# Kernel optimization log

Measured on AMD Instinct MI355X. Metric: run time of the kernel, lower is better.

## Reference

```python
import jax, jax.numpy as jnp
import numpy as np

B, N, D, H, DH = 2, 2048, 1024, 16, 64  # batch, seq, dim, heads, dim_head


def setup_inputs() -> dict:
    key = jax.random.key(0)
    ks = jax.random.split(key, 5)
    x = jax.random.normal(ks[0], (B, N, D), dtype=jnp.float32)
    Wq = jax.random.normal(ks[1], (D, H * DH), dtype=jnp.float32) * 0.02
    Wk = jax.random.normal(ks[2], (D, H * DH), dtype=jnp.float32) * 0.02
    Wv = jax.random.normal(ks[3], (D, H * DH), dtype=jnp.float32) * 0.02
    Wo = jax.random.normal(ks[4], (H * DH, D), dtype=jnp.float32) * 0.02
    bo = jnp.zeros((D,), dtype=jnp.float32)
    return {"x": x, "Wq": Wq, "Wk": Wk, "Wv": Wv, "Wo": Wo, "bo": bo}


def reference(x, Wq, Wk, Wv, Wo, bo):
    b, n, _ = x.shape
    scale = DH ** -0.5
    q = (x @ Wq).reshape(b, n, H, DH)
    k = (x @ Wk).reshape(b, n, H, DH)
    v = (x @ Wv).reshape(b, n, H, DH)
    # ALiBi slopes: 1 / (256**(1/H))**(h+1), per get_alibi_slope
    base = (2.0 ** 8) ** (1.0 / H)
    slope = 1.0 / base ** jnp.arange(1, H + 1, dtype=jnp.float32)  # [H]
    pos = jnp.arange(n, dtype=jnp.float32)
    # q_bias=[slope, slope*i], k_bias=[-j, 1] -> dot = slope*(i-j)
    bias = slope[:, None, None] * (pos[:, None] - pos[None, :])  # [H, N, N]
    scores = jnp.einsum('bihd,bjhd->bhij', q, k) * scale + bias[None]
    causal = pos[:, None] >= pos[None, :]  # i >= j
    scores = jnp.where(causal[None, None], scores, jnp.float32(-1e30))
    attn = jax.nn.softmax(scores, axis=-1)
    out = jnp.einsum('bhij,bjhd->bihd', attn, v).reshape(b, n, H * DH)
    return out @ Wo + bo
```

## Files before the change

kernel.cpp:

```cpp
#include <hip/hip_runtime.h>
#include <hip/hip_bf16.h>


typedef __bf16 bf16x8 __attribute__((ext_vector_type(8)));
typedef float f32x4 __attribute__((ext_vector_type(4)));
typedef short s4 __attribute__((ext_vector_type(4)));
typedef unsigned short ushort_t;

#define MFMA_16x16x32(a, b, c) __builtin_amdgcn_mfma_f32_16x16x32_bf16(a, b, c, 0, 0, 0)
#define MFMA16(a, b, c) __builtin_amdgcn_mfma_f32_16x16x16bf16_1k(a, b, c, 0, 0, 0)

__device__ __forceinline__ ushort_t f2bf(float f) {
    __hip_bfloat16 h = __float2bfloat16(f);
    return __builtin_bit_cast(ushort_t, h);
}
__device__ __forceinline__ float bf2f(ushort_t u) {
    unsigned x = ((unsigned)u) << 16;
    return __builtin_bit_cast(float, x);
}

__device__ __forceinline__ void gl_lds16(const ushort_t* g, ushort_t* l) {
    __builtin_amdgcn_global_load_lds(
        (const __attribute__((address_space(1))) void*)g,
        (__attribute__((address_space(3))) void*)l, 16, 0, 0);
}

__device__ __forceinline__ unsigned detect_fp32(const void* wp) {
    const ushort_t* w = (const ushort_t*)wp;
    unsigned c = 0;
    #pragma unroll
    for (int i = 0; i < 128; ++i) c += (((w[i] >> 7) & 0xFF) >= 0x7F) ? 1u : 0u;
    return (c > 8) ? 1u : 0u;
}

__device__ __forceinline__ uint4 load8(const void* p, size_t idx, unsigned flag) {
    if (flag) {
        const float* f = (const float*)p + idx;
        float4 a = *(const float4*)f;
        float4 b = *(const float4*)(f + 4);
        ushort_t u[8] = { f2bf(a.x), f2bf(a.y), f2bf(a.z), f2bf(a.w),
                          f2bf(b.x), f2bf(b.y), f2bf(b.z), f2bf(b.w) };
        return *(uint4*)u;
    }
    return *(const uint4*)((const ushort_t*)p + idx);
}

struct Sched { unsigned v[1536]; unsigned short pair[238]; };
constexpr Sched make_sched() {
    Sched s{};
    for (int i = 0; i < 1536; ++i) s.v[i] = 0;
    int jc[16] = {1, 1, 2, 2, 3, 4, 6, 8, 12, 16, 23, 32, 32, 32, 32, 32};
    int grp[8][4] = {
        {11, 12, 0, 2}, {13, 14, 1, 3}, {27, 28, 16, 18}, {29, 30, 17, 19},
        {15, 10, 5, 4}, {31, 26, 21, 20}, {9, 8, 7, 6}, {25, 24, 23, 22},
    };
    int np = 0;
    for (int x = 0; x < 8; ++x) {
        int sb_bh[200], sb_qb[200], sb_jb[200], sb_je[200], sb_kd[200], sb_k[200];
        int n = 0;
        for (int gi = 0; gi < 4; ++gi) {
            int bh = grp[x][gi], h = bh & 15;
            for (int qb = 0; qb < 32; ++qb) {
                int w = (qb + 1 < jc[h]) ? (qb + 1) : jc[h];
                if (w >= 16) {
                    int k = np++;
                    s.pair[k] = (unsigned short)((qb << 5) | bh);
                    int jm = w / 2;
                    sb_bh[n] = bh; sb_qb[n] = qb; sb_jb[n] = 0;  sb_je[n] = jm; sb_kd[n] = 2; sb_k[n] = k; ++n;
                    sb_bh[n] = bh; sb_qb[n] = qb; sb_jb[n] = jm; sb_je[n] = w;  sb_kd[n] = 3; sb_k[n] = k; ++n;
                } else {
                    sb_bh[n] = bh; sb_qb[n] = qb; sb_jb[n] = 0; sb_je[n] = w; sb_kd[n] = 1; sb_k[n] = 0; ++n;
                }
            }
        }
        int m = 0;
        for (int w = 16; w >= 1; --w)
            for (int i2 = 0; i2 < n; ++i2)
                if (sb_je[i2] - sb_jb[i2] == w) {
                    int t = m++;
                    int r = t >> 5, p = t & 31;
                    int cu = (r & 1) ? (31 - p) : p;
                    s.v[r * 256 + cu * 8 + x] = (unsigned)(
                        sb_kd[i2] | (sb_bh[i2] << 2) | (sb_qb[i2] << 7) |
                        (sb_jb[i2] << 12) | (sb_je[i2] << 17) | (sb_k[i2] << 23));
                }
    }
    return s;
}
__constant__ Sched g_sched = make_sched();

__global__ __launch_bounds__(256) void convert_x(
    const void* __restrict__ X, const void* __restrict__ Wq, const void* __restrict__ bo,
    ushort_t* __restrict__ Xc, ushort_t* __restrict__ boc)
{
    const unsigned flag = detect_fp32(Wq);
    const int blk = blockIdx.x;
    if (blk < 2048) {
        size_t idx = (size_t)blk * 2048 + (size_t)threadIdx.x * 8;
        *(uint4*)(Xc + idx) = load8(X, idx, flag);
    } else {
        size_t idx = (size_t)threadIdx.x * 8;
        if (idx < 1024) *(uint4*)(boc + idx) = load8(bo, idx, flag);
    }
}

__global__ __launch_bounds__(256) void transpose_w(
    const void* __restrict__ Wq, const void* __restrict__ Wk,
    const void* __restrict__ Wv, const void* __restrict__ Wo,
    ushort_t* __restrict__ WqT, ushort_t* __restrict__ WkT,
    ushort_t* __restrict__ WvT, ushort_t* __restrict__ WoT)
{
    __shared__ ushort_t T[64][72];
    const unsigned flag = detect_fp32(Wq);
    const int z = blockIdx.z;
    const void* W = (z == 0) ? Wq : ((z == 1) ? Wk : ((z == 2) ? Wv : Wo));
    ushort_t* WT = (z == 0) ? WqT : ((z == 1) ? WkT : ((z == 2) ? WvT : WoT));

    const int k0 = blockIdx.y * 64, n0 = blockIdx.x * 64;
    const int r = threadIdx.x >> 2, c = (threadIdx.x & 3) * 16;

    *(uint4*)&T[r][c]     = load8(W, (size_t)(k0 + r) * 1024 + n0 + c,     flag);
    *(uint4*)&T[r][c + 8] = load8(W, (size_t)(k0 + r) * 1024 + n0 + c + 8, flag);
    __syncthreads();
    ushort_t tmp[16];
    #pragma unroll
    for (int j = 0; j < 16; ++j) tmp[j] = T[c + j][r];
    *(uint4*)(WT + (size_t)(n0 + r) * 1024 + k0 + c)     = *(uint4*)&tmp[0];
    *(uint4*)(WT + (size_t)(n0 + r) * 1024 + k0 + c + 8) = *(uint4*)&tmp[8];
}

__global__ __launch_bounds__(256) void qkv_gemm(
    const ushort_t* __restrict__ X, const ushort_t* __restrict__ WqT,
    const ushort_t* __restrict__ WkT, const ushort_t* __restrict__ WvT,
    ushort_t* __restrict__ Q, ushort_t* __restrict__ K, ushort_t* __restrict__ Vt)
{
    __shared__ ushort_t As[128 * 32];
    __shared__ ushort_t Bs[128 * 32];

    const int z = blockIdx.z;
    const ushort_t* WT = (z == 0) ? WqT : ((z == 1) ? WkT : WvT);

    const int tid  = threadIdx.x;
    const int m0   = blockIdx.y * 128, n0 = blockIdx.x * 128;
    const int lane = tid & 63, wv = tid >> 6;
    const int quad = lane >> 4, l15 = lane & 15;
    const int wm = (wv & 1) * 64, wn = (wv >> 1) * 64;

    const int lrow = lane >> 2;
    const int schk = (lane & 3) ^ ((lane >> 3) & 3);
    const int ra0_ = wv * 16 + lrow;
    ushort_t* aB0 = As + wv * 512;
    ushort_t* aB1 = As + 2048 + wv * 512;
    ushort_t* bB0 = Bs + wv * 512;
    ushort_t* bB1 = Bs + 2048 + wv * 512;
    const int sp = quad ^ ((l15 >> 1) & 3);

    f32x4 acc[4][4] = {};

    for (int kt = 0; kt < 32; ++kt) {
        const int k0 = kt * 32;
        __syncthreads();
        gl_lds16(X  + (size_t)(m0 + ra0_)      * 1024 + k0 + schk * 8, aB0);
        gl_lds16(X  + (size_t)(m0 + 64 + ra0_) * 1024 + k0 + schk * 8, aB1);
        gl_lds16(WT + (size_t)(n0 + ra0_)      * 1024 + k0 + schk * 8, bB0);
        gl_lds16(WT + (size_t)(n0 + 64 + ra0_) * 1024 + k0 + schk * 8, bB1);
        __syncthreads();

        bf16x8 af[4], bfr[4];
        #pragma unroll
        for (int t = 0; t < 4; ++t) {
            af[t]  = *(const bf16x8*)(As + (wm + t * 16 + l15) * 32 + sp * 8);
            bfr[t] = *(const bf16x8*)(Bs + (wn + t * 16 + l15) * 32 + sp * 8);
        }
        #pragma unroll
        for (int mt = 0; mt < 4; ++mt)
            #pragma unroll
            for (int nt = 0; nt < 4; ++nt)
                acc[mt][nt] = MFMA_16x16x32(af[mt], bfr[nt], acc[mt][nt]);
    }

    #pragma unroll
    for (int mt = 0; mt < 4; ++mt) {
        #pragma unroll
        for (int nt = 0; nt < 4; ++nt) {
            if (z == 2) {
                int c  = n0 + wn + nt * 16 + l15;
                int h  = c >> 6, dh = c & 63;
                int mA = m0 + wm + mt * 16 + quad * 4;
                int b  = mA >> 11, nseq = mA & 2047;
                ushort_t pk[4];
                #pragma unroll
                for (int r = 0; r < 4; ++r) pk[r] = f2bf(acc[mt][nt][r]);
                *(ushort2*)(Vt + ((size_t)((b * 16 + h) * 64 + dh)) * 2048 + nseq)     = *(ushort2*)&pk[0];
                *(ushort2*)(Vt + ((size_t)((b * 16 + h) * 64 + dh)) * 2048 + nseq + 2) = *(ushort2*)&pk[2];
            } else {
                ushort_t* dst = (z == 0) ? Q : K;
                #pragma unroll
                for (int r = 0; r < 4; ++r) {
                    int m = m0 + wm + mt * 16 + quad * 4 + r;
                    int c = n0 + wn + nt * 16 + l15;
                    int b = m >> 11, nseq = m & 2047;
                    int h = c >> 6, dh = c & 63;
                    dst[((size_t)((b * 16 + h) * 2048 + nseq)) * 64 + dh] = f2bf(acc[mt][nt][r]);
                }
            }
        }
    }
}

__global__ __launch_bounds__(256) void attn_kernel(
    const ushort_t* __restrict__ Q, const ushort_t* __restrict__ K,
    const ushort_t* __restrict__ Vt, ushort_t* __restrict__ AO,
    float* __restrict__ partV, float* __restrict__ partL)
{
    __shared__ ushort_t Ks[64 * 72];
    __shared__ ushort_t Vs[64 * 72];

    const unsigned e = g_sched.v[blockIdx.x];
    const int kind = e & 3;
    if (kind == 0) return;

    const int tid  = threadIdx.x;
    const int wv   = tid >> 6, lane = tid & 63;
    const int quad = lane >> 4, l15 = lane & 15;
    const int bh   = (e >> 2) & 31, h = bh & 15, b = bh >> 4;
    const int qb   = (e >> 7) & 31;
    const int jbeg = (e >> 12) & 31;
    const int jend = (e >> 17) & 63;
    const int pk_  = (e >> 23) & 255;
    const int iw   = qb * 64 + wv * 16;
    const int i_   = iw + l15;

    const ushort_t* Qh = Q  + (size_t)bh * 2048 * 64;
    const ushort_t* Kh = K  + (size_t)bh * 2048 * 64;
    const ushort_t* Vh = Vt + (size_t)bh * 64 * 2048;

    const float LOG2E = 1.44269504088896340736f;
    const float sl2 = exp2f(-0.5f * (float)(h + 1)) * LOG2E;
    const float c1  = 0.125f * LOG2E;

    bf16x8 qf0 = *(const bf16x8*)(Qh + (size_t)(iw + l15) * 64 + quad * 8);
    bf16x8 qf1 = *(const bf16x8*)(Qh + (size_t)(iw + l15) * 64 + 32 + quad * 8);

    s4 onesf;
    #pragma unroll
    for (int e2 = 0; e2 < 4; ++e2) onesf[e2] = (short)0x3F80;

    float nb[4];
    #pragma unroll
    for (int r = 0; r < 4; ++r) nb[r] = -sl2 * (float)(quad * 4 + r);

    f32x4 accv[4] = {};
    f32x4 accl = {};

    const int sr = tid >> 2, sc = (tid & 3) * 16;

    const int j0b = jbeg * 64;
    uint4 ka0 = *(const uint4*)(Kh + (size_t)(j0b + sr) * 64 + sc);
    uint4 ka1 = *(const uint4*)(Kh + (size_t)(j0b + sr) * 64 + sc + 8);
    uint4 va0 = *(const uint4*)(Vh + (size_t)sr * 2048 + j0b + sc);
    uint4 va1 = *(const uint4*)(Vh + (size_t)sr * 2048 + j0b + sc + 8);

    auto subtile = [&](int jt, int js, bool masked) {
        const int j0s = jt * 64 + js * 16;
        const float bj = -sl2 * (float)j0s;
        f32x4 sT = {};
        bf16x8 kf0 = *(const bf16x8*)(Ks + (js * 16 + l15) * 72 + quad * 8);
        bf16x8 kf1 = *(const bf16x8*)(Ks + (js * 16 + l15) * 72 + 32 + quad * 8);
        sT = MFMA_16x16x32(kf0, qf0, sT);
        sT = MFMA_16x16x32(kf1, qf1, sT);
        unsigned u[4];
        #pragma unroll
        for (int r = 0; r < 4; ++r) {
            float p = exp2f(fmaf(sT[r], c1, nb[r] + bj));
            if (masked && (j0s + quad * 4 + r) > i_) p = 0.0f;
            u[r] = __builtin_bit_cast(unsigned, p) + 0x8000u;
        }
        uint2 dd = { (u[0] >> 16) | (u[1] & 0xFFFF0000u),
                     (u[2] >> 16) | (u[3] & 0xFFFF0000u) };
        s4 pf = __builtin_bit_cast(s4, dd);
        accl = MFMA16(onesf, pf, accl);
        #pragma unroll
        for (int dt = 0; dt < 4; ++dt) {
            s4 vf = *(const s4*)(Vs + (dt * 16 + l15) * 72 + js * 16 + quad * 4);
            accv[dt] = MFMA16(vf, pf, accv[dt]);
        }
    };

    for (int jt = jbeg; jt < jend; ++jt) {
        __syncthreads();
        *(uint4*)(Ks + sr * 72 + sc)     = ka0;
        *(uint4*)(Ks + sr * 72 + sc + 8) = ka1;
        *(uint4*)(Vs + sr * 72 + sc)     = va0;
        *(uint4*)(Vs + sr * 72 + sc + 8) = va1;
        __syncthreads();
        if (jt + 1 < jend) {
            int j0n = (jt + 1) * 64;
            ka0 = *(const uint4*)(Kh + (size_t)(j0n + sr) * 64 + sc);
            ka1 = *(const uint4*)(Kh + (size_t)(j0n + sr) * 64 + sc + 8);
            va0 = *(const uint4*)(Vh + (size_t)sr * 2048 + j0n + sc);
            va1 = *(const uint4*)(Vh + (size_t)sr * 2048 + j0n + sc + 8);
        }
        if (jt < qb) {
            #pragma unroll
            for (int js = 0; js < 4; ++js) subtile(jt, js, false);
        } else {
            for (int js = 0; js < wv; ++js) subtile(jt, js, false);
            subtile(jt, wv, true);
        }
    }

    if (kind == 1) {
        const float inv = 1.0f / fmaxf(accl[0], 1e-30f);
        const size_t obase = ((size_t)(b * 2048 + i_)) * 1024 + h * 64;
        #pragma unroll
        for (int dt = 0; dt < 4; ++dt) {
            ushort_t pk2[4];
            #pragma unroll
            for (int r = 0; r < 4; ++r) pk2[r] = f2bf(accv[dt][r] * inv);
            *(ushort2*)(AO + obase + dt * 16 + quad * 4)     = *(ushort2*)&pk2[0];
            *(ushort2*)(AO + obase + dt * 16 + quad * 4 + 2) = *(ushort2*)&pk2[2];
        }
    } else {
        const int ps = 2 * pk_ + (kind == 3 ? 1 : 0);
        const int rl = wv * 16 + l15;
        float* pv = partV + ((size_t)ps * 64 + rl) * 64;
        #pragma unroll
        for (int dt = 0; dt < 4; ++dt)
            *(f32x4*)(pv + dt * 16 + quad * 4) = accv[dt];
        partL[ps * 64 + rl] = accl[0];
    }
}

__global__ __launch_bounds__(256) void attn_merge(
    const float* __restrict__ partV, const float* __restrict__ partL,
    ushort_t* __restrict__ AO)
{
    const int p = blockIdx.x;
    const unsigned info = g_sched.pair[p];
    const int bh = info & 31, qb = info >> 5;
    const int b = bh >> 4, h = bh & 15;
    const int row = threadIdx.x >> 2, cg = (threadIdx.x & 3) * 16;

    const float* v0 = partV + ((size_t)(2 * p)     * 64 + row) * 64 + cg;
    const float* v1 = partV + ((size_t)(2 * p + 1) * 64 + row) * 64 + cg;
    const float l = partL[(2 * p) * 64 + row] + partL[(2 * p + 1) * 64 + row];
    const float inv = 1.0f / fmaxf(l, 1e-30f);

    ushort_t pk2[16];
    #pragma unroll
    for (int c = 0; c < 16; ++c) pk2[c] = f2bf((v0[c] + v1[c]) * inv);
    const size_t o = ((size_t)(b * 2048 + qb * 64 + row)) * 1024 + h * 64 + cg;
    *(uint4*)(AO + o)     = *(uint4*)&pk2[0];
    *(uint4*)(AO + o + 8) = *(uint4*)&pk2[8];
}

__global__ __launch_bounds__(256) void oproj_gemm(
    const ushort_t* __restrict__ A, const ushort_t* __restrict__ WT,
    const ushort_t* __restrict__ bias, float* __restrict__ out)
{
    __shared__ ushort_t As[128 * 32];
    __shared__ ushort_t Bs[128 * 32];

    const int tid  = threadIdx.x;
    const int m0   = blockIdx.y * 128, n0 = blockIdx.x * 128;
    const int lane = tid & 63, wv = tid >> 6;
    const int quad = lane >> 4, l15 = lane & 15;
    const int wm = (wv & 1) * 64, wn = (wv >> 1) * 64;

    const int lrow = lane >> 2;
    const int schk = (lane & 3) ^ ((lane >> 3) & 3);
    const int ra0_ = wv * 16 + lrow;
    ushort_t* aB0 = As + wv * 512;
    ushort_t* aB1 = As + 2048 + wv * 512;
    ushort_t* bB0 = Bs + wv * 512;
    ushort_t* bB1 = Bs + 2048 + wv * 512;
    const int sp = quad ^ ((l15 >> 1) & 3);

    f32x4 acc[4][4] = {};

    for (int kt = 0; kt < 32; ++kt) {
        const int k0 = kt * 32;
        __syncthreads();
        gl_lds16(A  + (size_t)(m0 + ra0_)      * 1024 + k0 + schk * 8, aB0);
        gl_lds16(A  + (size_t)(m0 + 64 + ra0_) * 1024 + k0 + schk * 8, aB1);
        gl_lds16(WT + (size_t)(n0 + ra0_)      * 1024 + k0 + schk * 8, bB0);
        gl_lds16(WT + (size_t)(n0 + 64 + ra0_) * 1024 + k0 + schk * 8, bB1);
        __syncthreads();

        bf16x8 af[4], bfr[4];
        #pragma unroll
        for (int t = 0; t < 4; ++t) {
            af[t]  = *(const bf16x8*)(As + (wm + t * 16 + l15) * 32 + sp * 8);
            bfr[t] = *(const bf16x8*)(Bs + (wn + t * 16 + l15) * 32 + sp * 8);
        }
        #pragma unroll
        for (int mt = 0; mt < 4; ++mt)
            #pragma unroll
            for (int nt = 0; nt < 4; ++nt)
                acc[mt][nt] = MFMA_16x16x32(af[mt], bfr[nt], acc[mt][nt]);
    }

    #pragma unroll
    for (int mt = 0; mt < 4; ++mt) {
        #pragma unroll
        for (int nt = 0; nt < 4; ++nt) {
            #pragma unroll
            for (int r = 0; r < 4; ++r) {
                int m = m0 + wm + mt * 16 + quad * 4 + r;
                int c = n0 + wn + nt * 16 + l15;
                out[(size_t)m * 1024 + c] = acc[mt][nt][r] + bf2f(bias[c]);
            }
        }
    }
}

extern "C" void kernel_launch(void* const* d_in, const int* in_sizes, int n_in,
                              void* d_out, int out_size, void* d_ws, size_t ws_size,
                              hipStream_t stream) {
    const void* X  = d_in[0];
    const void* Wq = d_in[1];
    const void* Wk = d_in[2];
    const void* Wv = d_in[3];
    const void* Wo = d_in[4];
    const void* bo = d_in[5];

    const size_t M = 1024 * 1024;
    ushort_t* ws  = (ushort_t*)d_ws;
    ushort_t* Qb  = ws;
    ushort_t* Kb  = ws + 4 * M;
    ushort_t* Vt  = ws + 8 * M;
    ushort_t* Xc  = ws + 12 * M;
    ushort_t* AO  = ws + 12 * M;
    ushort_t* WqT = ws + 16 * M;
    ushort_t* WkT = ws + 17 * M;
    ushort_t* WvT = ws + 18 * M;
    ushort_t* WoT = ws + 19 * M;
    ushort_t* boc = ws + 20 * M;
    float* partV  = (float*)(ws + 22 * M);
    float* partL  = partV + (size_t)476 * 64 * 64;
    float* out = (float*)d_out;

    convert_x<<<2049, 256, 0, stream>>>(X, Wq, bo, Xc, boc);
    transpose_w<<<dim3(16, 16, 4), 256, 0, stream>>>(Wq, Wk, Wv, Wo, WqT, WkT, WvT, WoT);
    qkv_gemm<<<dim3(8, 32, 3), 256, 0, stream>>>(Xc, WqT, WkT, WvT, Qb, Kb, Vt);
    attn_kernel<<<1536, 256, 0, stream>>>(Qb, Kb, Vt, AO, partV, partL);
    attn_merge<<<238, 256, 0, stream>>>(partV, partL, AO);
    oproj_gemm<<<dim3(8, 32), 256, 0, stream>>>(AO, WoT, boc, out);
}
```

Measured before the change: 178.8 us.

## Split long attention rows into up-to-8-tile chunks and fuse prep kernels

The attention schedule now splits any query block with 9 or more key tiles into chunks of at most 8 tiles, where it used to split only blocks of 16 or more, and only in two. The merge kernel sums a variable number of partial results. This is meant to shrink the longest work item and balance load across CUs. The input conversion and weight transpose kernels are fused into one launch to save launch overhead. The cost is more partial-result traffic, more blocks and a larger partV workspace.

```diff
diff --git a/kernel.cpp b/kernel.cpp
--- a/kernel.cpp
+++ b/kernel.cpp
@@ -45,88 +45,91 @@
     return *(const uint4*)((const ushort_t*)p + idx);
 }
 
-struct Sched { unsigned v[1536]; unsigned short pair[238]; };
+struct Sched { unsigned v[1792]; unsigned mi[384]; };
 constexpr Sched make_sched() {
     Sched s{};
-    for (int i = 0; i < 1536; ++i) s.v[i] = 0;
+    for (int i = 0; i < 1792; ++i) s.v[i] = 0;
+    for (int i = 0; i < 384; ++i) s.mi[i] = 0;
     int jc[16] = {1, 1, 2, 2, 3, 4, 6, 8, 12, 16, 23, 32, 32, 32, 32, 32};
     int grp[8][4] = {
         {11, 12, 0, 2}, {13, 14, 1, 3}, {27, 28, 16, 18}, {29, 30, 17, 19},
         {15, 10, 5, 4}, {31, 26, 21, 20}, {9, 8, 7, 6}, {25, 24, 23, 22},
     };
-    int np = 0;
+    int nslot = 0, nmi = 0;
     for (int x = 0; x < 8; ++x) {
-        int sb_bh[200], sb_qb[200], sb_jb[200], sb_je[200], sb_kd[200], sb_k[200];
+        int sb_bh[256], sb_qb[256], sb_jb[256], sb_je[256], sb_sl[256];
         int n = 0;
         for (int gi = 0; gi < 4; ++gi) {
             int bh = grp[x][gi], h = bh & 15;
             for (int qb = 0; qb < 32; ++qb) {
                 int w = (qb + 1 < jc[h]) ? (qb + 1) : jc[h];
-                if (w >= 16) {
-                    int k = np++;
-                    s.pair[k] = (unsigned short)((qb << 5) | bh);
-                    int jm = w / 2;
-                    sb_bh[n] = bh; sb_qb[n] = qb; sb_jb[n] = 0;  sb_je[n] = jm; sb_kd[n] = 2; sb_k[n] = k; ++n;
-                    sb_bh[n] = bh; sb_qb[n] = qb; sb_jb[n] = jm; sb_je[n] = w;  sb_kd[n] = 3; sb_k[n] = k; ++n;
+                if (w >= 9) {
+                    int nch = (w + 7) / 8;
+                    s.mi[nmi++] = (unsigned)(bh | (qb << 5) | (nslot << 10) | (nch << 21));
+                    int jb = 0;
+                    for (int c = 0; c < nch; ++c) {
+                        int je = jb + (w - jb) / (nch - c)
+                               + (((w - jb) % (nch - c)) ? 1 : 0);
+                        sb_bh[n] = bh; sb_qb[n] = qb; sb_jb[n] = jb;
+                        sb_je[n] = je; sb_sl[n] = nslot++; ++n;
+                        jb = je;
+                    }
                 } else {
-                    sb_bh[n] = bh; sb_qb[n] = qb; sb_jb[n] = 0; sb_je[n] = w; sb_kd[n] = 1; sb_k[n] = 0; ++n;
+                    sb_bh[n] = bh; sb_qb[n] = qb; sb_jb[n] = 0;
+                    sb_je[n] = w; sb_sl[n] = 2047; ++n;
                 }
             }
         }
         int m = 0;
-        for (int w = 16; w >= 1; --w)
+        for (int w = 8; w >= 1; --w)
             for (int i2 = 0; i2 < n; ++i2)
                 if (sb_je[i2] - sb_jb[i2] == w) {
                     int t = m++;
                     int r = t >> 5, p = t & 31;
                     int cu = (r & 1) ? (31 - p) : p;
                     s.v[r * 256 + cu * 8 + x] = (unsigned)(
-                        sb_kd[i2] | (sb_bh[i2] << 2) | (sb_qb[i2] << 7) |
-                        (sb_jb[i2] << 12) | (sb_je[i2] << 17) | (sb_k[i2] << 23));
+                        sb_bh[i2] | (sb_qb[i2] << 5) | (sb_jb[i2] << 10) |
+                        (sb_je[i2] << 15) | (sb_sl[i2] << 21));
                 }
     }
     return s;
 }
 __constant__ Sched g_sched = make_sched();
 
-__global__ __launch_bounds__(256) void convert_x(
-    const void* __restrict__ X, const void* __restrict__ Wq, const void* __restrict__ bo,
-    ushort_t* __restrict__ Xc, ushort_t* __restrict__ boc)
+__global__ __launch_bounds__(256) void prep(
+    const void* __restrict__ X, const void* __restrict__ Wq,
+    const void* __restrict__ Wk, const void* __restrict__ Wv,
+    const void* __restrict__ Wo, const void* __restrict__ bo,
+    ushort_t* __restrict__ Xc, ushort_t* __restrict__ boc,
+    ushort_t* __restrict__ WqT, ushort_t* __restrict__ WkT,
+    ushort_t* __restrict__ WvT, ushort_t* __restrict__ WoT)
 {
+    __shared__ ushort_t T[64][72];
     const unsigned flag = detect_fp32(Wq);
     const int blk = blockIdx.x;
     if (blk < 2048) {
         size_t idx = (size_t)blk * 2048 + (size_t)threadIdx.x * 8;
         *(uint4*)(Xc + idx) = load8(X, idx, flag);
-    } else {
+    } else if (blk == 2048) {
         size_t idx = (size_t)threadIdx.x * 8;
         if (idx < 1024) *(uint4*)(boc + idx) = load8(bo, idx, flag);
-    }
-}
-
-__global__ __launch_bounds__(256) void transpose_w(
-    const void* __restrict__ Wq, const void* __restrict__ Wk,
-    const void* __restrict__ Wv, const void* __restrict__ Wo,
-    ushort_t* __restrict__ WqT, ushort_t* __restrict__ WkT,
-    ushort_t* __restrict__ WvT, ushort_t* __restrict__ WoT)
-{
-    __shared__ ushort_t T[64][72];
-    const unsigned flag = detect_fp32(Wq);
-    const int z = blockIdx.z;
-    const void* W = (z == 0) ? Wq : ((z == 1) ? Wk : ((z == 2) ? Wv : Wo));
-    ushort_t* WT = (z == 0) ? WqT : ((z == 1) ? WkT : ((z == 2) ? WvT : WoT));
-
-    const int k0 = blockIdx.y * 64, n0 = blockIdx.x * 64;
-    const int r = threadIdx.x >> 2, c = (threadIdx.x & 3) * 16;
-
-    *(uint4*)&T[r][c]     = load8(W, (size_t)(k0 + r) * 1024 + n0 + c,     flag);
-    *(uint4*)&T[r][c + 8] = load8(W, (size_t)(k0 + r) * 1024 + n0 + c + 8, flag);
-    __syncthreads();
-    ushort_t tmp[16];
-    #pragma unroll
-    for (int j = 0; j < 16; ++j) tmp[j] = T[c + j][r];
-    *(uint4*)(WT + (size_t)(n0 + r) * 1024 + k0 + c)     = *(uint4*)&tmp[0];
-    *(uint4*)(WT + (size_t)(n0 + r) * 1024 + k0 + c + 8) = *(uint4*)&tmp[8];
+    } else {
+        const int t = blk - 2049;
+        const int z = t >> 8;
+        const void* W = (z == 0) ? Wq : ((z == 1) ? Wk : ((z == 2) ? Wv : Wo));
+        ushort_t* WT = (z == 0) ? WqT : ((z == 1) ? WkT : ((z == 2) ? WvT : WoT));
+        const int k0 = ((t >> 4) & 15) * 64, n0 = (t & 15) * 64;
+        const int r = threadIdx.x >> 2, c = (threadIdx.x & 3) * 16;
+
+        *(uint4*)&T[r][c]     = load8(W, (size_t)(k0 + r) * 1024 + n0 + c,     flag);
+        *(uint4*)&T[r][c + 8] = load8(W, (size_t)(k0 + r) * 1024 + n0 + c + 8, flag);
+        __syncthreads();
+        ushort_t tmp[16];
+        #pragma unroll
+        for (int j = 0; j < 16; ++j) tmp[j] = T[c + j][r];
+        *(uint4*)(WT + (size_t)(n0 + r) * 1024 + k0 + c)     = *(uint4*)&tmp[0];
+        *(uint4*)(WT + (size_t)(n0 + r) * 1024 + k0 + c + 8) = *(uint4*)&tmp[8];
+    }
 }
 
 __global__ __launch_bounds__(256) void qkv_gemm(
@@ -217,17 +220,16 @@
     __shared__ ushort_t Vs[64 * 72];
 
     const unsigned e = g_sched.v[blockIdx.x];
-    const int kind = e & 3;
-    if (kind == 0) return;
+    const int jend = (e >> 15) & 63;
+    if (jend == 0) return;
 
     const int tid  = threadIdx.x;
     const int wv   = tid >> 6, lane = tid & 63;
     const int quad = lane >> 4, l15 = lane & 15;
-    const int bh   = (e >> 2) & 31, h = bh & 15, b = bh >> 4;
-    const int qb   = (e >> 7) & 31;
-    const int jbeg = (e >> 12) & 31;
-    const int jend = (e >> 17) & 63;
-    const int pk_  = (e >> 23) & 255;
+    const int bh   = e & 31, h = bh & 15, b = bh >> 4;
+    const int qb   = (e >> 5) & 31;
+    const int jbeg = (e >> 10) & 31;
+    const int slot = (e >> 21) & 2047;
     const int iw   = qb * 64 + wv * 16;
     const int i_   = iw + l15;
 
@@ -310,7 +312,7 @@
         }
     }
 
-    if (kind == 1) {
+    if (slot == 2047) {
         const float inv = 1.0f / fmaxf(accl[0], 1e-30f);
         const size_t obase = ((size_t)(b * 2048 + i_)) * 1024 + h * 64;
         #pragma unroll
@@ -322,13 +324,12 @@
             *(ushort2*)(AO + obase + dt * 16 + quad * 4 + 2) = *(ushort2*)&pk2[2];
         }
     } else {
-        const int ps = 2 * pk_ + (kind == 3 ? 1 : 0);
         const int rl = wv * 16 + l15;
-        float* pv = partV + ((size_t)ps * 64 + rl) * 64;
+        float* pv = partV + ((size_t)slot * 64 + rl) * 64;
         #pragma unroll
         for (int dt = 0; dt < 4; ++dt)
             *(f32x4*)(pv + dt * 16 + quad * 4) = accv[dt];
-        partL[ps * 64 + rl] = accl[0];
+        partL[slot * 64 + rl] = accl[0];
     }
 }
 
@@ -336,20 +337,25 @@
     const float* __restrict__ partV, const float* __restrict__ partL,
     ushort_t* __restrict__ AO)
 {
-    const int p = blockIdx.x;
-    const unsigned info = g_sched.pair[p];
-    const int bh = info & 31, qb = info >> 5;
+    const unsigned info = g_sched.mi[blockIdx.x];
+    const int bh = info & 31, qb = (info >> 5) & 31;
+    const int base = (info >> 10) & 2047, cnt = (info >> 21) & 7;
     const int b = bh >> 4, h = bh & 15;
     const int row = threadIdx.x >> 2, cg = (threadIdx.x & 3) * 16;
 
-    const float* v0 = partV + ((size_t)(2 * p)     * 64 + row) * 64 + cg;
-    const float* v1 = partV + ((size_t)(2 * p + 1) * 64 + row) * 64 + cg;
-    const float l = partL[(2 * p) * 64 + row] + partL[(2 * p + 1) * 64 + row];
+    float acc[16] = {};
+    float l = 0.0f;
+    for (int c = 0; c < cnt; ++c) {
+        const float* v = partV + ((size_t)(base + c) * 64 + row) * 64 + cg;
+        #pragma unroll
+        for (int j = 0; j < 16; ++j) acc[j] += v[j];
+        l += partL[(base + c) * 64 + row];
+    }
     const float inv = 1.0f / fmaxf(l, 1e-30f);
 
     ushort_t pk2[16];
     #pragma unroll
-    for (int c = 0; c < 16; ++c) pk2[c] = f2bf((v0[c] + v1[c]) * inv);
+    for (int j = 0; j < 16; ++j) pk2[j] = f2bf(acc[j] * inv);
     const size_t o = ((size_t)(b * 2048 + qb * 64 + row)) * 1024 + h * 64 + cg;
     *(uint4*)(AO + o)     = *(uint4*)&pk2[0];
     *(uint4*)(AO + o + 8) = *(uint4*)&pk2[8];
@@ -438,13 +444,12 @@
     ushort_t* WoT = ws + 19 * M;
     ushort_t* boc = ws + 20 * M;
     float* partV  = (float*)(ws + 22 * M);
-    float* partL  = partV + (size_t)476 * 64 * 64;
+    float* partL  = partV + (size_t)1040 * 64 * 64;
     float* out = (float*)d_out;
 
-    convert_x<<<2049, 256, 0, stream>>>(X, Wq, bo, Xc, boc);
-    transpose_w<<<dim3(16, 16, 4), 256, 0, stream>>>(Wq, Wk, Wv, Wo, WqT, WkT, WvT, WoT);
+    prep<<<3073, 256, 0, stream>>>(X, Wq, Wk, Wv, Wo, bo, Xc, boc, WqT, WkT, WvT, WoT);
     qkv_gemm<<<dim3(8, 32, 3), 256, 0, stream>>>(Xc, WqT, WkT, WvT, Qb, Kb, Vt);
-    attn_kernel<<<1536, 256, 0, stream>>>(Qb, Kb, Vt, AO, partV, partL);
-    attn_merge<<<238, 256, 0, stream>>>(partV, partL, AO);
+    attn_kernel<<<1792, 256, 0, stream>>>(Qb, Kb, Vt, AO, partV, partL);
+    attn_merge<<<384, 256, 0, stream>>>(partV, partL, AO);
     oproj_gemm<<<dim3(8, 32), 256, 0, stream>>>(AO, WoT, boc, out);
 }
```

After: 176.1 us. About the same (-1.5%).
